# Optimization experiments

Measured on AMD Instinct MI355X. Metric: run time of the kernel, lower is better.

## Reference

```python
import jax, jax.numpy as jnp
import numpy as np

EPS = 1e-7
MAX_NORM = 10.0  # safe_expmap tangent-norm clamp


def _sinh_div(d):
    # sinh(d)/d, stable at d->0
    ds = jnp.maximum(d, 1e-6)
    return jnp.where(d < 1e-6, 1.0, jnp.sinh(ds) / ds)


def _div_sinh(d):
    # d/sinh(d), stable at d->0
    ds = jnp.maximum(d, 1e-6)
    return jnp.where(d < 1e-6, 1.0, ds / jnp.sinh(ds))


def projx(x):
    # re-project onto hyperboloid: x0 = sqrt(1 + ||x_spatial||^2)
    sp = x[..., 1:]
    x0 = jnp.sqrt(1.0 + jnp.sum(sp * sp, -1, keepdims=True))
    return jnp.concatenate([x0, sp], -1)


def logmap0(x):
    # log map at origin o=(1,0,...,0); tangent has first coord 0
    x0 = jnp.clip(x[..., :1], 1.0 + EPS, None)
    d = jnp.arccosh(x0)
    v_sp = _div_sinh(d) * x[..., 1:]
    return jnp.concatenate([jnp.zeros_like(x0), v_sp], -1)


def safe_expmap0(v):
    # exp map at origin with norm clamping for stability
    sp = v[..., 1:]
    n = jnp.sqrt(jnp.sum(sp * sp, -1, keepdims=True))
    scale = jnp.minimum(1.0, MAX_NORM / jnp.maximum(n, EPS))
    sp = sp * scale
    m = jnp.minimum(n, MAX_NORM)
    return jnp.concatenate([jnp.cosh(m), _sinh_div(m) * sp], -1)


def lorentz_inner(x, y):
    return -x[..., :1] * y[..., :1] + jnp.sum(x[..., 1:] * y[..., 1:], -1, keepdims=True)


def logmap(x, y):
    ip = jnp.clip(lorentz_inner(x, y), None, -(1.0 + EPS))
    d = jnp.arccosh(-ip)
    return _div_sinh(d) * (y + ip * x)


def safe_expmap(x, v):
    # exp map at x with Lorentz-norm clamping
    vv = lorentz_inner(v, v)
    n = jnp.sqrt(jnp.clip(vv, 0.0, None))
    scale = jnp.minimum(1.0, MAX_NORM / jnp.maximum(n, EPS))
    v = v * scale
    m = jnp.minimum(n, MAX_NORM)
    return jnp.cosh(m) * x + _sinh_div(m) * v


def lorentz_linear(x_hyp, W, b):
    # Lorentz -> tangent -> linear -> Lorentz
    y_tan = logmap0(x_hyp) @ W.T + b
    return projx(safe_expmap0(y_tan))


def setup_inputs() -> dict:
    key = jax.random.key(0)
    ks = jax.random.split(key, 8)
    N, D, H = 32768, 256, 1024
    z_sp = 0.5 * jax.random.normal(ks[0], (N, D - 1), dtype=jnp.float32)
    z_h = projx(jnp.concatenate([jnp.zeros((N, 1), jnp.float32), z_sp], -1))
    s = lambda fi, fo: (2.0 / (fi + fo)) ** 0.5
    return {
        "z_h": z_h,
        "w0": s(D, H) * jax.random.normal(ks[1], (H, D), dtype=jnp.float32),
        "b0": jnp.zeros((H,), jnp.float32),
        "w1": s(H, H) * jax.random.normal(ks[2], (H, H), dtype=jnp.float32),
        "b1": jnp.zeros((H,), jnp.float32),
        "w2": s(H, D) * jax.random.normal(ks[3], (D, H), dtype=jnp.float32),
        "b2": jnp.zeros((D,), jnp.float32),
        "alpha": jnp.float32(0.7),
        "step_size": jnp.float32(1.0),
    }


def reference(z_h, w0, b0, w1, b1, w2, b2, alpha, step_size):
    # v_tangent branch: x_previous is None, average_velocity is None
    v_tangent = logmap0(z_h)
    v_hyp = projx(safe_expmap0(v_tangent))

    # LorentzMLP (n_layers=2 -> 3 LorentzLinear layers); dropout is identity (eval)
    x = v_hyp
    for W, b in ((w0, b0), (w1, b1)):
        x = lorentz_linear(x, W, b)
        x = projx(safe_expmap0(logmap0(x)))
    v_transformed_hyp = lorentz_linear(x, w2, b2)

    v_transformed = logmap0(v_transformed_hyp)
    step = jax.nn.sigmoid(step_size)
    v_final = step * v_transformed
    z_update = projx(safe_expmap(z_h, v_final))

    a = jax.nn.sigmoid(alpha)
    tangent_direction = logmap(z_h, z_update)
    scaled_tangent = (1.0 - a) * tangent_direction
    z_next = projx(safe_expmap(z_h, scaled_tangent))
    return (z_next, z_h)
```

## Files before the change

### kernel.cpp

```cpp
#include <hip/hip_runtime.h>
#include <math.h>

#define EPSF 1e-7f
#define MAXN 10.0f

typedef unsigned short ushortT;
typedef __bf16 bf16_8 __attribute__((ext_vector_type(8)));
typedef float f32_4 __attribute__((ext_vector_type(4)));

#define MFMA16 __builtin_amdgcn_mfma_f32_16x16x32_bf16
#define BAR asm volatile("s_barrier" ::: "memory")

__device__ __forceinline__ float sinh_div_f(float d) {
    float ds = fmaxf(d, 1e-6f);
    return (d < 1e-6f) ? 1.0f : sinhf(ds) / ds;
}
__device__ __forceinline__ float div_sinh_f(float d) {
    float ds = fmaxf(d, 1e-6f);
    return (d < 1e-6f) ? 1.0f : ds / sinhf(ds);
}
__device__ __forceinline__ float wred(float v) {
#pragma unroll
    for (int off = 32; off > 0; off >>= 1) v += __shfl_xor(v, off, 64);
    return v;
}
__device__ __forceinline__ float red16(float v) {
    v += __shfl_xor(v, 1, 64); v += __shfl_xor(v, 2, 64);
    v += __shfl_xor(v, 4, 64); v += __shfl_xor(v, 8, 64);
    return v;
}
__device__ __forceinline__ void bsplit(float x, ushortT& h, ushortT& l) {
    unsigned u = __float_as_uint(x);
    unsigned r = (u + 0x7fffu + ((u >> 16) & 1u)) >> 16;
    h = (ushortT)r;
    float lo = x - __uint_as_float(r << 16);
    unsigned ul = __float_as_uint(lo);
    l = (ushortT)((ul + 0x7fffu + ((ul >> 16) & 1u)) >> 16);
}
__device__ __forceinline__ void gload_lds16(const void* g, void* l) {
    __builtin_amdgcn_global_load_lds(
        (const __attribute__((address_space(1))) unsigned int*)g,
        (__attribute__((address_space(3))) unsigned int*)l, 16, 0, 0);
}
__device__ __forceinline__ void split_item(const float* __restrict__ x,
                                           ushortT* __restrict__ hi, ushortT* __restrict__ lo,
                                           int idx) {
    float4 v = reinterpret_cast<const float4*>(x)[idx];
    float f[4] = {v.x, v.y, v.z, v.w};
    ushortT hh[4], ll[4];
#pragma unroll
    for (int e = 0; e < 4; ++e) bsplit(f[e], hh[e], ll[e]);
    reinterpret_cast<ushort4*>(hi)[idx] = ushort4{hh[0], hh[1], hh[2], hh[3]};
    reinterpret_cast<ushort4*>(lo)[idx] = ushort4{ll[0], ll[1], ll[2], ll[3]};
}

__global__ void combo1(const float* __restrict__ z, const float* __restrict__ w0,
                       const float* __restrict__ w1,
                       ushortT* __restrict__ p0h, ushortT* __restrict__ p0l,
                       ushortT* __restrict__ w0h, ushortT* __restrict__ w0l,
                       ushortT* __restrict__ w1h, ushortT* __restrict__ w1l, int N) {
    int b = blockIdx.x, tid = threadIdx.x;
    if (b < 256) {
        split_item(w0, w0h, w0l, b * 256 + tid);
        return;
    }
    if (b < 1280) {
        split_item(w1, w1h, w1l, (b - 256) * 256 + tid);
        return;
    }
    int gw = (b - 1280) * 4 + (tid >> 6);
    int lane = tid & 63;
    if (gw >= N) return;
    float4 zv = reinterpret_cast<const float4*>(z + (size_t)gw * 256)[lane];
    float z0 = __shfl(zv.x, 0, 64);
    float x0 = fmaxf(z0, 1.f + EPSF);
    float d = acoshf(x0);
    float f = div_sinh_f(d);
    float vx = (lane == 0) ? 0.f : zv.x * f;
    float vy = zv.y * f, vz = zv.z * f, vw = zv.w * f;
    float ss = wred(vx * vx + vy * vy + vz * vz + vw * vw);
    float n = sqrtf(ss);
    float s = fminf(1.f, MAXN / fmaxf(n, EPSF));
    float o[4] = {vx * s, vy * s, vz * s, vw * s};
    ushortT hh[4], ll[4];
#pragma unroll
    for (int e = 0; e < 4; ++e) bsplit(o[e], hh[e], ll[e]);
    reinterpret_cast<ushort4*>(p0h + (size_t)gw * 256)[lane] = ushort4{hh[0], hh[1], hh[2], hh[3]};
    reinterpret_cast<ushort4*>(p0l + (size_t)gw * 256)[lane] = ushort4{ll[0], ll[1], ll[2], ll[3]};
}

__global__ void rowscale_kernel(const float* __restrict__ partials, float* __restrict__ scale,
                                int N, int nSlices) {
    int r = blockIdx.x * blockDim.x + threadIdx.x;
    if (r >= N) return;
    float s = 0.f;
    for (int k = 0; k < nSlices; ++k) s += partials[(size_t)k * N + r];
    float n = sqrtf(s);
    scale[r] = fminf(1.f, MAXN / fmaxf(n, EPSF));
}

__global__ void combo2(const float* __restrict__ partials, float* __restrict__ s2,
                       const float* __restrict__ w2,
                       ushortT* __restrict__ w2h, ushortT* __restrict__ w2l, int N) {
    int b = blockIdx.x, tid = threadIdx.x;
    if (b < 128) {
        int r = b * 256 + tid;
        if (r >= N) return;
        float s = 0.f;
        for (int k = 0; k < 16; ++k) s += partials[(size_t)k * N + r];
        float n = sqrtf(s);
        s2[r] = fminf(1.f, MAXN / fmaxf(n, EPSF));
        return;
    }
    split_item(w2, w2h, w2l, (b - 128) * 256 + tid);
}

template<int OUTMODE, int IM>
__global__ __launch_bounds__(512, 2) void gemm_v8(
    const ushortT* __restrict__ Ah_g, const ushortT* __restrict__ Al_g,
    const ushortT* __restrict__ Wh_g, const ushortT* __restrict__ Wl_g,
    const float* __restrict__ bias, const float* __restrict__ scaleA,
    float* __restrict__ outF, ushortT* __restrict__ outH, ushortT* __restrict__ outL,
    float* __restrict__ partials, int K, int M, int nColBlk, int Nrows,
    const float* __restrict__ z_g, const float* __restrict__ alpha_p,
    const float* __restrict__ step_p)
{
    constexpr int BM = IM * 32;
    constexpr int AS = BM * 32;
    constexpr int BS = 256 * 32;
    constexpr int BUF = 2 * AS + 2 * BS;
    constexpr int HM = IM / 2;
    __shared__ __align__(16) ushortT lds[2 * BUF];

    const int tid = threadIdx.x;
    const int wid = tid >> 6, lane = tid & 63;
    const int nwg = gridDim.x;
    const int swz = ((int)blockIdx.x & 7) * (nwg >> 3) + ((int)blockIdx.x >> 3);
    const int rb = swz / nColBlk, cb = swz % nColBlk;
    const int rowBase = rb * BM, colBase = cb * 256;

    const int rl = tid >> 2;
    const int ks = (tid & 3) ^ ((rl >> 1) & 3);
    const int d8 = tid * 8;
    const ushortT* gAh0 = Ah_g + (size_t)(rowBase + rl) * K + ks * 8;
    const ushortT* gAl0 = Al_g + (size_t)(rowBase + rl) * K + ks * 8;
    const ushortT* gAh1 = Ah_g + (size_t)(rowBase + 128 + rl) * K + ks * 8;
    const ushortT* gAl1 = Al_g + (size_t)(rowBase + 128 + rl) * K + ks * 8;
    const ushortT* gBh0 = Wh_g + (size_t)(colBase + rl) * K + ks * 8;
    const ushortT* gBh1 = Wh_g + (size_t)(colBase + 128 + rl) * K + ks * 8;
    const ushortT* gBl0 = Wl_g + (size_t)(colBase + rl) * K + ks * 8;
    const ushortT* gBl1 = Wl_g + (size_t)(colBase + 128 + rl) * K + ks * 8;
#define STG(p, dst, nbo, nk) gload_lds16((p) + (nk), &lds[(nbo) + (dst) + d8])

    const int warpM = wid >> 2, warpN = wid & 3;
    const int frow = lane & 15, fk = lane >> 4;
    const int pslot8 = (fk ^ ((frow >> 1) & 3)) * 8;
    const int aoff = (warpM * (IM * 16) + frow) * 32 + pslot8;
    const int boff = (warpN * 64 + frow) * 32 + pslot8;

    f32_4 acc[IM][4];
#pragma unroll
    for (int i = 0; i < IM; ++i)
#pragma unroll
        for (int j = 0; j < 4; ++j) acc[i][j] = f32_4{0.f, 0.f, 0.f, 0.f};

    STG(gAh0, 0, 0, 0);
    if constexpr (IM == 8) STG(gAh1, 4096, 0, 0);
    STG(gAl0, AS, 0, 0);
    if constexpr (IM == 8) STG(gAl1, AS + 4096, 0, 0);
    STG(gBh0, 2 * AS, 0, 0); STG(gBh1, 2 * AS + 4096, 0, 0);
    STG(gBl0, 2 * AS + BS, 0, 0); STG(gBl1, 2 * AS + BS + 4096, 0, 0);
    asm volatile("s_waitcnt vmcnt(0)" ::: "memory");
    BAR;

    const int nt = K >> 5;
    for (int t = 0; t < nt; ++t) {
        const ushortT* lb = &lds[(t & 1) * BUF];
        const int nbo = ((t & 1) ^ 1) * BUF;
        const int nk = (t + 1) << 5;
        const bool more = (t + 1) < nt;
        bf16_8 ah[IM], bh[4], bl[4], al[IM];

#pragma unroll
        for (int i = 0; i < IM; ++i) ah[i] = *reinterpret_cast<const bf16_8*>(&lb[aoff + i * 512]);
#pragma unroll
        for (int j = 0; j < 4; ++j) bh[j] = *reinterpret_cast<const bf16_8*>(&lb[2 * AS + boff + j * 512]);
        if (more) { STG(gAh0, 0, nbo, nk); if constexpr (IM == 8) STG(gAh1, 4096, nbo, nk); }
        __builtin_amdgcn_s_setprio(1);
#pragma unroll
        for (int i = 0; i < HM; ++i)
#pragma unroll
            for (int j = 0; j < 4; ++j) acc[i][j] = MFMA16(ah[i], bh[j], acc[i][j], 0, 0, 0);
        __builtin_amdgcn_s_setprio(0);
        if (more) {
            if constexpr (IM == 8) asm volatile("s_waitcnt vmcnt(2)" ::: "memory");
            else                   asm volatile("s_waitcnt vmcnt(1)" ::: "memory");
        } else {
            asm volatile("s_waitcnt vmcnt(0)" ::: "memory");
        }
        BAR;

#pragma unroll
        for (int j = 0; j < 4; ++j) bl[j] = *reinterpret_cast<const bf16_8*>(&lb[2 * AS + BS + boff + j * 512]);
        if (more) { STG(gAl0, AS, nbo, nk); if constexpr (IM == 8) STG(gAl1, AS + 4096, nbo, nk); }
        __builtin_amdgcn_s_setprio(1);
#pragma unroll
        for (int i = HM; i < IM; ++i)
#pragma unroll
            for (int j = 0; j < 4; ++j) acc[i][j] = MFMA16(ah[i], bh[j], acc[i][j], 0, 0, 0);
        __builtin_amdgcn_s_setprio(0);
        BAR;

#pragma unroll
        for (int i = 0; i < HM; ++i) al[i] = *reinterpret_cast<const bf16_8*>(&lb[AS + aoff + i * 512]);
        if (more) { STG(gBh0, 2 * AS, nbo, nk); STG(gBh1, 2 * AS + 4096, nbo, nk); }
        __builtin_amdgcn_s_setprio(1);
#pragma unroll
        for (int i = 0; i < HM; ++i)
#pragma unroll
            for (int j = 0; j < 4; ++j) acc[i][j] = MFMA16(ah[i], bl[j], acc[i][j], 0, 0, 0);
        __builtin_amdgcn_s_setprio(0);
        BAR;

#pragma unroll
        for (int i = HM; i < IM; ++i) al[i] = *reinterpret_cast<const bf16_8*>(&lb[AS + aoff + i * 512]);
        if (more) { STG(gBl0, 2 * AS + BS, nbo, nk); STG(gBl1, 2 * AS + BS + 4096, nbo, nk); }
        __builtin_amdgcn_s_setprio(1);
#pragma unroll
        for (int i = HM; i < IM; ++i)
#pragma unroll
            for (int j = 0; j < 4; ++j) acc[i][j] = MFMA16(ah[i], bl[j], acc[i][j], 0, 0, 0);
        __builtin_amdgcn_s_setprio(0);
        BAR;

        __builtin_amdgcn_s_setprio(1);
#pragma unroll
        for (int i = 0; i < HM; ++i)
#pragma unroll
            for (int j = 0; j < 4; ++j) acc[i][j] = MFMA16(al[i], bh[j], acc[i][j], 0, 0, 0);
#pragma unroll
        for (int i = HM; i < IM; ++i)
#pragma unroll
            for (int j = 0; j < 4; ++j) acc[i][j] = MFMA16(al[i], bh[j], acc[i][j], 0, 0, 0);
        __builtin_amdgcn_s_setprio(0);
        asm volatile("s_waitcnt vmcnt(2)" ::: "memory");
        BAR;
    }
#undef STG

    const int cbase = colBase + warpN * 64 + frow;
    if constexpr (OUTMODE == 0) {
        float bv[4];
#pragma unroll
        for (int j = 0; j < 4; ++j) bv[j] = bias[cbase + j * 16];
        const size_t slice = (size_t)(cb * 4 + warpN) * Nrows;
#pragma unroll
        for (int i = 0; i < IM; ++i) {
            const int row0 = rowBase + warpM * (IM * 16) + i * 16 + fk * 4;
            float4 sa4 = float4{1.f, 1.f, 1.f, 1.f};
            if (scaleA) sa4 = *reinterpret_cast<const float4*>(&scaleA[row0]);
            float psum[4];
#pragma unroll
            for (int r = 0; r < 4; ++r) {
                const float sa = reinterpret_cast<const float*>(&sa4)[r];
                const int row = row0 + r;
                const size_t base = (size_t)row * M;
                float ssv = 0.f;
#pragma unroll
                for (int j = 0; j < 4; ++j) {
                    float y = sa * acc[i][j][r] + bv[j];
                    if (j == 0 && cbase == 0) y = 0.f;
                    ushortT h, l;
                    bsplit(y, h, l);
                    outH[base + cbase + j * 16] = h;
                    outL[base + cbase + j * 16] = l;
                    ssv += y * y;
                }
                psum[r] = red16(ssv);
            }
            if (frow == 0) {
#pragma unroll
                for (int r = 0; r < 4; ++r) partials[slice + row0 + r] = psum[r];
            }
        }
    }
    if constexpr (OUTMODE == 2) {
        float* red  = (float*)&lds[0];
        float* bufZ = red;
        float* bufA = red + 128;
        float* bufB = red + 640;
        float* bufC = red + 1664;
        float* bufD = red + 2176;
        const float stepv = 1.f / (1.f + expf(-step_p[0]));
        const float av    = 1.f / (1.f + expf(-alpha_p[0]));
        const int cb0 = warpN * 64 + frow;
        const bool c0own = (cb0 == 0);
        float bv[4];
#pragma unroll
        for (int j = 0; j < 4; ++j) bv[j] = bias[cb0 + j * 16];
        BAR;
#pragma unroll
        for (int ig = 0; ig < 2; ++ig) {
            float yv[2][4][4], zz[2][4][4], z0[2][4], st0[2][4];
#pragma unroll
            for (int ii = 0; ii < 2; ++ii) {
                const int i = ig * 2 + ii;
                const int row0 = warpM * 64 + i * 16 + fk * 4;
                float4 sa4 = float4{1.f, 1.f, 1.f, 1.f};
                if (scaleA) sa4 = *reinterpret_cast<const float4*>(&scaleA[rowBase + row0]);
#pragma unroll
                for (int rr = 0; rr < 4; ++rr) {
                    const float sa = reinterpret_cast<const float*>(&sa4)[rr];
                    const size_t gz = (size_t)(rowBase + row0 + rr) * 256 + cb0;
#pragma unroll
                    for (int j = 0; j < 4; ++j) {
                        yv[ii][j][rr] = sa * acc[i][j][rr] + bv[j];
                        zz[ii][j][rr] = z_g[gz + j * 16];
                    }
                }
            }
#pragma unroll
            for (int ii = 0; ii < 2; ++ii) {
                const int row0 = warpM * 64 + (ig * 2 + ii) * 16 + fk * 4;
#pragma unroll
                for (int rr = 0; rr < 4; ++rr) {
                    float p = 0.f;
#pragma unroll
                    for (int j = 0; j < 4; ++j) {
                        float yq = (c0own && j == 0) ? 0.f : yv[ii][j][rr];
                        p += yq * yq;
                    }
                    p = red16(p);
                    if (frow == 0) bufA[(row0 + rr) * 4 + warpN] = p;
                    if (c0own) bufZ[row0 + rr] = zz[ii][0][rr];
                }
            }
            BAR;
#pragma unroll
            for (int ii = 0; ii < 2; ++ii) {
                const int row0 = warpM * 64 + (ig * 2 + ii) * 16 + fk * 4;
#pragma unroll
                for (int rr = 0; rr < 4; ++rr) {
                    const int rw = row0 + rr;
                    float ss2 = bufA[rw * 4] + bufA[rw * 4 + 1] + bufA[rw * 4 + 2] + bufA[rw * 4 + 3];
                    z0[ii][rr] = bufZ[rw];
                    float n2 = sqrtf(ss2);
                    float k1 = fminf(1.f, MAXN / fmaxf(n2, EPSF)) * stepv;
                    float n  = k1 * n2;
                    float scv = fminf(1.f, MAXN / fmaxf(n, EPSF));
                    float m  = fminf(n, MAXN);
                    float ch = coshf(m), sdv = sinh_div_f(m);
                    float pe = 0.f, pz = 0.f;
#pragma unroll
                    for (int j = 0; j < 4; ++j) {
                        float vf = (c0own && j == 0) ? 0.f : yv[ii][j][rr] * k1;
                        float e  = ch * zz[ii][j][rr] + sdv * scv * vf;
                        yv[ii][j][rr] = e;
                        if (!(c0own && j == 0)) { pe += e * e; pz += zz[ii][j][rr] * e; }
                    }
                    pe = red16(pe); pz = red16(pz);
                    if (frow == 0) { bufB[rw * 8 + warpN * 2] = pe; bufB[rw * 8 + warpN * 2 + 1] = pz; }
                }
            }
            BAR;
#pragma unroll
            for (int ii = 0; ii < 2; ++ii) {
                const int row0 = warpM * 64 + (ig * 2 + ii) * 16 + fk * 4;
#pragma unroll
                for (int rr = 0; rr < 4; ++rr) {
                    const int rw = row0 + rr;
                    float r3 = bufB[rw * 8] + bufB[rw * 8 + 2] + bufB[rw * 8 + 4] + bufB[rw * 8 + 6];
                    float r4 = bufB[rw * 8 + 1] + bufB[rw * 8 + 3] + bufB[rw * 8 + 5] + bufB[rw * 8 + 7];
                    float u0 = sqrtf(1.f + r3);
                    float ip = fminf(r4 - z0[ii][rr] * u0, -(1.f + EPSF));
                    float dd = acoshf(-ip);
                    float g = div_sinh_f(dd);
                    float oa = (1.f - av) * g;
                    st0[ii][rr] = oa * (u0 + ip * z0[ii][rr]);
                    float p5 = 0.f;
#pragma unroll
                    for (int j = 0; j < 4; ++j) {
                        float st = oa * (yv[ii][j][rr] + ip * zz[ii][j][rr]);
                        yv[ii][j][rr] = st;
                        if (!(c0own && j == 0)) p5 += st * st;
                    }
                    p5 = red16(p5);
                    if (frow == 0) bufC[rw * 4 + warpN] = p5;
                }
            }
            BAR;
#pragma unroll
            for (int ii = 0; ii < 2; ++ii) {
                const int row0 = warpM * 64 + (ig * 2 + ii) * 16 + fk * 4;
#pragma unroll
                for (int rr = 0; rr < 4; ++rr) {
                    const int rw = row0 + rr;
                    float r5 = bufC[rw * 4] + bufC[rw * 4 + 1] + bufC[rw * 4 + 2] + bufC[rw * 4 + 3];
                    float vv2 = r5 - st0[ii][rr] * st0[ii][rr];
                    float n5 = sqrtf(fmaxf(vv2, 0.f));
                    float s5 = fminf(1.f, MAXN / fmaxf(n5, EPSF));
                    float m5 = fminf(n5, MAXN);
                    float ch5 = coshf(m5), sd5 = sinh_div_f(m5);
                    float p6 = 0.f;
#pragma unroll
                    for (int j = 0; j < 4; ++j) {
                        float f = ch5 * zz[ii][j][rr] + sd5 * s5 * yv[ii][j][rr];
                        yv[ii][j][rr] = f;
                        if (!(c0own && j == 0)) p6 += f * f;
                    }
                    p6 = red16(p6);
                    if (frow == 0) bufD[rw * 4 + warpN] = p6;
                }
            }
            BAR;
#pragma unroll
            for (int ii = 0; ii < 2; ++ii) {
                const int row0 = warpM * 64 + (ig * 2 + ii) * 16 + fk * 4;
#pragma unroll
                for (int rr = 0; rr < 4; ++rr) {
                    const int rw = row0 + rr;
                    float r6 = bufD[rw * 4] + bufD[rw * 4 + 1] + bufD[rw * 4 + 2] + bufD[rw * 4 + 3];
                    float zn0 = sqrtf(1.f + r6);
                    const size_t rowG = (size_t)(rowBase + rw);
#pragma unroll
                    for (int j = 0; j < 4; ++j) {
                        const int col = cb0 + j * 16;
                        float v = (c0own && j == 0) ? zn0 : yv[ii][j][rr];
                        outF[rowG * 256 + col] = v;
                        outF[((size_t)Nrows + rowG) * 256 + col] = zz[ii][j][rr];
                    }
                }
            }
        }
    }
}

extern "C" void kernel_launch(void* const* d_in, const int* in_sizes, int n_in,
                              void* d_out, int out_size, void* d_ws, size_t ws_size,
                              hipStream_t stream) {
    const float* z_h  = (const float*)d_in[0];
    const float* w0   = (const float*)d_in[1];
    const float* b0   = (const float*)d_in[2];
    const float* w1   = (const float*)d_in[3];
    const float* b1   = (const float*)d_in[4];
    const float* w2   = (const float*)d_in[5];
    const float* b2   = (const float*)d_in[6];
    const float* alph = (const float*)d_in[7];
    const float* stps = (const float*)d_in[8];
    float* out = (float*)d_out;

    const int D = 256, H = 1024;
    const int N = in_sizes[0] / D;

    char* ob = (char*)d_out;
    ushortT* p0h = (ushortT*)ob;
    ushortT* p0l = (ushortT*)(ob + 16777216);
    char* s2b = ob + 33554432;
    ushortT* w0h = (ushortT*)(s2b);
    ushortT* w0l = (ushortT*)(s2b + 524288);
    ushortT* w1h = (ushortT*)(s2b + 1048576);
    ushortT* w1l = (ushortT*)(s2b + 3145728);
    float* partials = (float*)(s2b + 5242880);
    float* s1 = (float*)(s2b + 7340032);

    ushortT* paH = (ushortT*)d_ws;
    ushortT* paL = paH + (size_t)N * H;
    ushortT* pbH = paL + (size_t)N * H;
    ushortT* pbL = pbH + (size_t)N * H;
    ushortT* w2h = (ushortT*)d_ws;
    ushortT* w2l = (ushortT*)((char*)d_ws + 524288);
    float* s2 = (float*)((char*)d_ws + 1048576);

    combo1<<<1280 + N / 4, 256, 0, stream>>>(z_h, w0, w1, p0h, p0l, w0h, w0l, w1h, w1l, N);

    gemm_v8<0, 8><<<(N / 256) * (H / 256), 512, 0, stream>>>(
        p0h, p0l, w0h, w0l, b0, nullptr, nullptr, paH, paL, partials, D, H, H / 256, N,
        nullptr, nullptr, nullptr);
    rowscale_kernel<<<(N + 255) / 256, 256, 0, stream>>>(partials, s1, N, 16);

    gemm_v8<0, 8><<<(N / 256) * (H / 256), 512, 0, stream>>>(
        paH, paL, w1h, w1l, b1, s1, nullptr, pbH, pbL, partials, H, H, H / 256, N,
        nullptr, nullptr, nullptr);

    combo2<<<384, 256, 0, stream>>>(partials, s2, w2, w2h, w2l, N);

    gemm_v8<2, 4><<<(N / 128) * (D / 256), 512, 0, stream>>>(
        pbH, pbL, w2h, w2l, b2, s2, out, nullptr, nullptr, nullptr, H, D, D / 256, N,
        z_h, alph, stps);
}
```

Measured before the change: 390.4 us.

## Issue all next-tile global loads upfront and drop intra-iteration barriers

The GEMM main loop changes from a four-phase schedule, where each phase issues part of the next tile's global-to-LDS loads and ends with a barrier, to one that issues every prefetch at the top of the iteration. It then runs all three MFMA passes (hi*hi, hi*lo, lo*hi) back to back and waits for all loads with a single barrier at the end. The aim is fewer barriers and more memory-level parallelism per iteration. In exchange, the interleaving of loads with compute is lost, register pressure rises because all al fragments are held at once, and there is a full vmcnt(0) stall before the barrier.

```diff
diff --git a/kernel.cpp b/kernel.cpp
--- a/kernel.cpp
+++ b/kernel.cpp
@@ -116,7 +116,7 @@
 }
 
 template<int OUTMODE, int IM>
-__global__ __launch_bounds__(512, 2) void gemm_v8(
+__global__ __launch_bounds__(512, 2) void gemm_v9(
     const ushortT* __restrict__ Ah_g, const ushortT* __restrict__ Al_g,
     const ushortT* __restrict__ Wh_g, const ushortT* __restrict__ Wl_g,
     const float* __restrict__ bias, const float* __restrict__ scaleA,
@@ -179,71 +179,47 @@
         const int nbo = ((t & 1) ^ 1) * BUF;
         const int nk = (t + 1) << 5;
         const bool more = (t + 1) < nt;
+
+        if (more) {
+            STG(gAh0, 0, nbo, nk);
+            if constexpr (IM == 8) STG(gAh1, 4096, nbo, nk);
+            STG(gAl0, AS, nbo, nk);
+            if constexpr (IM == 8) STG(gAl1, AS + 4096, nbo, nk);
+            STG(gBh0, 2 * AS, nbo, nk); STG(gBh1, 2 * AS + 4096, nbo, nk);
+            STG(gBl0, 2 * AS + BS, nbo, nk); STG(gBl1, 2 * AS + BS + 4096, nbo, nk);
+        }
+
         bf16_8 ah[IM], bh[4], bl[4], al[IM];
-
 #pragma unroll
         for (int i = 0; i < IM; ++i) ah[i] = *reinterpret_cast<const bf16_8*>(&lb[aoff + i * 512]);
 #pragma unroll
         for (int j = 0; j < 4; ++j) bh[j] = *reinterpret_cast<const bf16_8*>(&lb[2 * AS + boff + j * 512]);
-        if (more) { STG(gAh0, 0, nbo, nk); if constexpr (IM == 8) STG(gAh1, 4096, nbo, nk); }
         __builtin_amdgcn_s_setprio(1);
 #pragma unroll
-        for (int i = 0; i < HM; ++i)
+        for (int i = 0; i < IM; ++i)
 #pragma unroll
             for (int j = 0; j < 4; ++j) acc[i][j] = MFMA16(ah[i], bh[j], acc[i][j], 0, 0, 0);
         __builtin_amdgcn_s_setprio(0);
-        if (more) {
-            if constexpr (IM == 8) asm volatile("s_waitcnt vmcnt(2)" ::: "memory");
-            else                   asm volatile("s_waitcnt vmcnt(1)" ::: "memory");
-        } else {
-            asm volatile("s_waitcnt vmcnt(0)" ::: "memory");
-        }
-        BAR;
 
 #pragma unroll
         for (int j = 0; j < 4; ++j) bl[j] = *reinterpret_cast<const bf16_8*>(&lb[2 * AS + BS + boff + j * 512]);
-        if (more) { STG(gAl0, AS, nbo, nk); if constexpr (IM == 8) STG(gAl1, AS + 4096, nbo, nk); }
         __builtin_amdgcn_s_setprio(1);
 #pragma unroll
-        for (int i = HM; i < IM; ++i)
-#pragma unroll
-            for (int j = 0; j < 4; ++j) acc[i][j] = MFMA16(ah[i], bh[j], acc[i][j], 0, 0, 0);
-        __builtin_amdgcn_s_setprio(0);
-        BAR;
-
-#pragma unroll
-        for (int i = 0; i < HM; ++i) al[i] = *reinterpret_cast<const bf16_8*>(&lb[AS + aoff + i * 512]);
-        if (more) { STG(gBh0, 2 * AS, nbo, nk); STG(gBh1, 2 * AS + 4096, nbo, nk); }
-        __builtin_amdgcn_s_setprio(1);
-#pragma unroll
-        for (int i = 0; i < HM; ++i)
+        for (int i = 0; i < IM; ++i)
 #pragma unroll
             for (int j = 0; j < 4; ++j) acc[i][j] = MFMA16(ah[i], bl[j], acc[i][j], 0, 0, 0);
         __builtin_amdgcn_s_setprio(0);
-        BAR;
-
-#pragma unroll
-        for (int i = HM; i < IM; ++i) al[i] = *reinterpret_cast<const bf16_8*>(&lb[AS + aoff + i * 512]);
-        if (more) { STG(gBl0, 2 * AS + BS, nbo, nk); STG(gBl1, 2 * AS + BS + 4096, nbo, nk); }
+
+#pragma unroll
+        for (int i = 0; i < IM; ++i) al[i] = *reinterpret_cast<const bf16_8*>(&lb[AS + aoff + i * 512]);
         __builtin_amdgcn_s_setprio(1);
 #pragma unroll
-        for (int i = HM; i < IM; ++i)
-#pragma unroll
-            for (int j = 0; j < 4; ++j) acc[i][j] = MFMA16(ah[i], bl[j], acc[i][j], 0, 0, 0);
-        __builtin_amdgcn_s_setprio(0);
-        BAR;
-
-        __builtin_amdgcn_s_setprio(1);
-#pragma unroll
-        for (int i = 0; i < HM; ++i)
-#pragma unroll
-            for (int j = 0; j < 4; ++j) acc[i][j] = MFMA16(al[i], bh[j], acc[i][j], 0, 0, 0);
-#pragma unroll
-        for (int i = HM; i < IM; ++i)
+        for (int i = 0; i < IM; ++i)
 #pragma unroll
             for (int j = 0; j < 4; ++j) acc[i][j] = MFMA16(al[i], bh[j], acc[i][j], 0, 0, 0);
         __builtin_amdgcn_s_setprio(0);
-        asm volatile("s_waitcnt vmcnt(2)" ::: "memory");
+
+        asm volatile("s_waitcnt vmcnt(0)" ::: "memory");
         BAR;
     }
 #undef STG
@@ -473,18 +449,18 @@
 
     combo1<<<1280 + N / 4, 256, 0, stream>>>(z_h, w0, w1, p0h, p0l, w0h, w0l, w1h, w1l, N);
 
-    gemm_v8<0, 8><<<(N / 256) * (H / 256), 512, 0, stream>>>(
+    gemm_v9<0, 8><<<(N / 256) * (H / 256), 512, 0, stream>>>(
         p0h, p0l, w0h, w0l, b0, nullptr, nullptr, paH, paL, partials, D, H, H / 256, N,
         nullptr, nullptr, nullptr);
     rowscale_kernel<<<(N + 255) / 256, 256, 0, stream>>>(partials, s1, N, 16);
 
-    gemm_v8<0, 8><<<(N / 256) * (H / 256), 512, 0, stream>>>(
+    gemm_v9<0, 8><<<(N / 256) * (H / 256), 512, 0, stream>>>(
         paH, paL, w1h, w1l, b1, s1, nullptr, pbH, pbL, partials, H, H, H / 256, N,
         nullptr, nullptr, nullptr);
 
     combo2<<<384, 256, 0, stream>>>(partials, s2, w2, w2h, w2l, N);
 
-    gemm_v8<2, 4><<<(N / 128) * (D / 256), 512, 0, stream>>>(
+    gemm_v9<2, 4><<<(N / 128) * (D / 256), 512, 0, stream>>>(
         pbH, pbL, w2h, w2l, b2, s2, out, nullptr, nullptr, nullptr, H, D, D / 256, N,
         z_h, alph, stps);
 }
```

New measurement: 394.8 us. About the same (+1.1%).
